# Performance work log

Hardware: AMD Instinct MI355X
Metric: run time of the kernel (lower is better)

Reference implementation:

```python
import jax, jax.numpy as jnp
import numpy as np

N_NODES = 50000
N_EDGES = 800000
F_IN = 2
T = 12
HID = 64
OUT = 12
K = 2  # diffusion order: identity + 1-hop (out- and in-directed)


def setup_inputs() -> dict:
    key = jax.random.key(0)
    ks = jax.random.split(key, 12)
    inp = {}
    inp["x"] = jax.random.normal(ks[0], (1, N_NODES, F_IN, T), dtype=jnp.float32)
    inp["edge_index"] = jax.random.randint(ks[1], (2, N_EDGES), 0, N_NODES)
    inp["edge_weight"] = jax.random.uniform(ks[2], (N_EDGES,), dtype=jnp.float32)

    def u(k, shape, fan):
        s = 1.0 / np.sqrt(fan)
        return jax.random.uniform(k, shape, jnp.float32, -s, s)

    c1 = F_IN + HID   # 66: DCRNN gates operate on cat([X, H])
    c2 = HID + HID    # 128
    inp["w1z"] = u(ks[3], (2, K, c1, HID), c1); inp["b1z"] = jnp.zeros((HID,), jnp.float32)
    inp["w1r"] = u(ks[4], (2, K, c1, HID), c1); inp["b1r"] = jnp.zeros((HID,), jnp.float32)
    inp["w1h"] = u(ks[5], (2, K, c1, HID), c1); inp["b1h"] = jnp.zeros((HID,), jnp.float32)
    inp["w2z"] = u(ks[6], (2, K, c2, HID), c2); inp["b2z"] = jnp.zeros((HID,), jnp.float32)
    inp["w2r"] = u(ks[7], (2, K, c2, HID), c2); inp["b2r"] = jnp.zeros((HID,), jnp.float32)
    inp["w2h"] = u(ks[8], (2, K, c2, HID), c2); inp["b2h"] = jnp.zeros((HID,), jnp.float32)
    inp["lin_w"] = u(ks[9], (HID, OUT), HID)
    inp["lin_b"] = u(ks[10], (OUT,), HID)
    return inp


def _dconv(X, row, col, norm_out, norm_in, w, b):
    # K=2 diffusion conv: H = X@W[:,0] + (D_O^-1 W diffusion)@W[0,1] + (D_I^-1 W^T diffusion)@W[1,1] + b
    H = X @ w[0, 0] + X @ w[1, 0]
    Xr = X[row]  # gather source-node features per edge: [E, C]
    Tx_o = jax.ops.segment_sum(norm_out[:, None] * Xr, col, num_segments=N_NODES)
    Tx_i = jax.ops.segment_sum(norm_in[:, None] * Xr, col, num_segments=N_NODES)
    return H + Tx_o @ w[0, 1] + Tx_i @ w[1, 1] + b


def _cell(X, H, row, col, no, ni, wz, bz, wr, br, wh, bh):
    # GRU-style DCRNN cell
    XH = jnp.concatenate([X, H], axis=1)
    Z = jax.nn.sigmoid(_dconv(XH, row, col, no, ni, wz, bz))
    R = jax.nn.sigmoid(_dconv(XH, row, col, no, ni, wr, br))
    Ht = jnp.tanh(_dconv(jnp.concatenate([X, R * H], axis=1), row, col, no, ni, wh, bh))
    return Z * H + (1.0 - Z) * Ht


def reference(x, edge_index, edge_weight, w1z, b1z, w1r, b1r, w1h, b1h,
              w2z, b2z, w2r, b2r, w2h, b2h, lin_w, lin_b):
    row, col = edge_index[0], edge_index[1]
    deg_out = jax.ops.segment_sum(edge_weight, row, num_segments=N_NODES)
    deg_in = jax.ops.segment_sum(edge_weight, col, num_segments=N_NODES)
    norm_out = edge_weight / deg_out[row]  # per-edge weight of D_O^{-1} W
    norm_in = edge_weight / deg_in[col]    # per-edge weight of D_I^{-1} W^T
    xs = jnp.transpose(x[0], (2, 0, 1))    # [T, N, F] (batch = 1)

    def step(carry, xt):
        h1, h2 = carry
        h1 = jax.nn.relu(_cell(xt, h1, row, col, norm_out, norm_in, w1z, b1z, w1r, b1r, w1h, b1h))
        h2 = jax.nn.relu(_cell(h1, h2, row, col, norm_out, norm_in, w2z, b2z, w2r, b2r, w2h, b2h))
        return (h1, h2), None

    h0 = jnp.zeros((N_NODES, HID), x.dtype)
    (h1, h2), _ = jax.lax.scan(step, (h0, h0), xs)
    out = h2 @ lin_w + lin_b  # [N, 12]
    return out.reshape(1, N_NODES, OUT)
```

## Files before the change

### kernel.cpp

```cpp
#include <hip/hip_runtime.h>

#define NN 50000
#define NE 800000
#define TT 12
#define NBIN (4 * NN)
#define NBLK ((NBIN + 255) / 256)

typedef _Float16 h16;
typedef __attribute__((ext_vector_type(2))) _Float16 h16x2;
typedef __attribute__((ext_vector_type(4))) _Float16 h16x4;
typedef __attribute__((ext_vector_type(8))) _Float16 half8;
typedef __attribute__((ext_vector_type(4))) float f32x4;
typedef __attribute__((address_space(3))) h16 as3h16;
typedef __attribute__((address_space(3))) half8 as3half8;

static constexpr size_t alignup(size_t x) { return (x + 255) & ~(size_t)255; }
static constexpr size_t O_CNT  = 0;
static constexpr size_t O_CUR  = alignup(O_CNT + NBIN + 1);
static constexpr size_t O_DEGO = alignup(O_CUR + NBIN);
static constexpr size_t O_BSUM = alignup(O_DEGO + NN);
static constexpr size_t O_BEXC = O_BSUM + 1024;
static constexpr size_t O_EDG  = alignup(O_BEXC + 1024);
static constexpr size_t O_TXX  = alignup(O_EDG + (size_t)NE * 2);
static constexpr size_t O_WF1ZR= alignup(O_TXX + (size_t)TT * NN * 4);
static constexpr size_t O_WF1H = alignup(O_WF1ZR + 12288);
static constexpr size_t O_WF2ZR= alignup(O_WF1H + 6144);
static constexpr size_t O_WF2H = alignup(O_WF2ZR + 24576);
static constexpr size_t O_WX1ZR= alignup(O_WF2H + 12288);
static constexpr size_t O_WX1H = alignup(O_WX1ZR + 768);
static constexpr size_t O_PX0  = alignup(O_WX1H + 384);
static constexpr size_t O_PX1  = O_PX0 + (size_t)NN * 64;
static constexpr size_t O_PZR  = O_PX1 + (size_t)NN * 64;
static constexpr size_t O_Z1   = O_PZR + (size_t)NN * 64;
static constexpr size_t O_Z2   = O_Z1 + (size_t)NN * 32;
static constexpr size_t O_TXA  = alignup(O_Z2 + (size_t)NN * 32);
static constexpr size_t O_TXB  = alignup(O_TXA + (size_t)NN * 64);
static constexpr size_t WS_FLOATS = O_TXB + (size_t)NN * 128;

__device__ __forceinline__ float sigm_(float x) { return 1.f / (1.f + __expf(-x)); }
__device__ __forceinline__ float tanh_(float x) { float e = __expf(2.f * x); return 1.f - 2.f / (e + 1.f); }

__device__ __forceinline__ void gld_lds16(const h16* g, as3h16* l) {
    __builtin_amdgcn_global_load_lds(
        (const __attribute__((address_space(1))) void*)g,
        (__attribute__((address_space(3))) void*)l, 16, 0, 0);
}

template <int N>
__device__ __forceinline__ void wait_lgkm0_vm() {
    if constexpr (N == 0)      asm volatile("s_waitcnt lgkmcnt(0) vmcnt(0)" ::: "memory");
    else if constexpr (N == 1) asm volatile("s_waitcnt lgkmcnt(0) vmcnt(1)" ::: "memory");
    else                       asm volatile("s_waitcnt lgkmcnt(0) vmcnt(2)" ::: "memory");
}


__global__ __launch_bounds__(256) void k_zero(float* ws) {
    size_t i = (size_t)blockIdx.x * 256 + threadIdx.x;
    size_t stride = (size_t)gridDim.x * 256;
    for (size_t p = i; p < O_BSUM + 2048; p += stride) ((int*)ws)[p] = 0;
    for (size_t p = i; p < (size_t)NN * 128; p += stride) ws[O_PX0 + p] = 0.f;
    for (size_t p = i; p < (size_t)NN * 128; p += stride) ws[O_TXB + p] = 0.f;
}

__global__ __launch_bounds__(256) void k_hist(const int* ei, float* ws) {
    int e = blockIdx.x * 256 + threadIdx.x;
    if (e >= NE) return;
    int r = ei[e], c = ei[NE + e];
    int bin = c * 4 + r / 12500;
    int rk = atomicAdd((int*)ws + O_CNT + bin, 1);
    ((int*)ws)[O_TXX + e] = rk;
}

__global__ __launch_bounds__(256) void k_scanA(float* ws) {
    __shared__ int sh[256];
    int t = threadIdx.x, i = blockIdx.x * 256 + t;
    int v = (i < NBIN) ? ((int*)ws)[O_CNT + i] : 0;
    sh[t] = v; __syncthreads();
    for (int o = 128; o > 0; o >>= 1) { if (t < o) sh[t] += sh[t + o]; __syncthreads(); }
    if (t == 0) ((int*)ws)[O_BSUM + blockIdx.x] = sh[0];
}

__global__ __launch_bounds__(256) void k_scanB(float* ws) {
    __shared__ int tot[256];
    int t = threadIdx.x;
    int* bsum = (int*)ws + O_BSUM;
    int* bexc = (int*)ws + O_BEXC;
    int base = t * 4;
    int v0 = (base + 0 < NBLK) ? bsum[base + 0] : 0;
    int v1 = (base + 1 < NBLK) ? bsum[base + 1] : 0;
    int v2 = (base + 2 < NBLK) ? bsum[base + 2] : 0;
    int v3 = (base + 3 < NBLK) ? bsum[base + 3] : 0;
    int sum = v0 + v1 + v2 + v3;
    tot[t] = sum; __syncthreads();
    for (int o = 1; o < 256; o <<= 1) {
        int a = (t >= o) ? tot[t - o] : 0;
        __syncthreads(); tot[t] += a; __syncthreads();
    }
    int excl = tot[t] - sum;
    if (base + 0 < NBLK) bexc[base + 0] = excl;
    if (base + 1 < NBLK) bexc[base + 1] = excl + v0;
    if (base + 2 < NBLK) bexc[base + 2] = excl + v0 + v1;
    if (base + 3 < NBLK) bexc[base + 3] = excl + v0 + v1 + v2;
    if (t == 255) ((int*)ws)[O_CNT + NBIN] = tot[255];
}

__global__ __launch_bounds__(256) void k_scanC(float* ws) {
    __shared__ int sh[256];
    int t = threadIdx.x, b = blockIdx.x, i = b * 256 + t;
    int v = (i < NBIN) ? ((int*)ws)[O_CNT + i] : 0;
    sh[t] = v; __syncthreads();
    for (int o = 1; o < 256; o <<= 1) {
        int a = (t >= o) ? sh[t - o] : 0;
        __syncthreads(); sh[t] += a; __syncthreads();
    }
    if (i < NBIN) ((int*)ws)[O_CNT + i] = ((int*)ws)[O_BEXC + b] + sh[t] - v;
}

__global__ __launch_bounds__(256) void k_scatter(const int* ei, const float* ew, float* ws) {
    int e = blockIdx.x * 256 + threadIdx.x;
    if (e >= NE) return;
    int r = ei[e], c = ei[NE + e];
    float w = ew[e];
    atomicAdd(ws + O_DEGO + r, w);
    int bin = c * 4 + r / 12500;
    int p = ((const int*)ws)[O_CNT + bin] + ((const int*)ws)[O_TXX + e];
    uint2 rec; rec.x = (unsigned)r; rec.y = __float_as_uint(w);
    ((uint2*)(ws + O_EDG))[p] = rec;
}

__global__ __launch_bounds__(256) void k_norm(float* ws) {
    int n = blockIdx.x * 4 + (threadIdx.x >> 6);
    int lane = threadIdx.x & 63;
    const int* offs = (const int*)ws + O_CNT;
    uint2* recs = (uint2*)(ws + O_EDG);
    const float* dego = ws + O_DEGO;
    int e0 = offs[4 * n], e1 = offs[4 * n + 4];
    float s = 0.f;
    for (int e = e0 + lane; e < e1; e += 64) s += __uint_as_float(recs[e].y);
    #pragma unroll
    for (int m = 1; m < 64; m <<= 1) s += __shfl_xor(s, m);
    float inv = 1.f / s;
    for (int e = e0 + lane; e < e1; e += 64) {
        uint2 r = recs[e];
        float w = __uint_as_float(r.y);
        h16x2 nv; nv.x = (h16)(w / dego[r.x]); nv.y = (h16)(w * inv);
        r.y = __builtin_bit_cast(unsigned int, nv);
        recs[e] = r;
    }
}

__global__ __launch_bounds__(256) void k_aggx(const float* __restrict__ x, float* __restrict__ ws) {
    int tid = threadIdx.x;
    int n = blockIdx.x * 8 + (tid >> 5);
    int l = tid & 31;
    const int* offs = (const int*)ws + O_CNT;
    const uint2* recs = (const uint2*)(ws + O_EDG);
    int e0 = offs[4 * n], e1 = offs[4 * n + 4];
    int f = l / 12, tt2 = l % 12;
    bool act = l < 24;
    float ao = 0.f, ai = 0.f;
    uint2 rc0, rc1;
    if (e0 < e1) {
        rc0 = recs[e0];
        rc1 = recs[(e0 + 1 < e1) ? e0 + 1 : e1 - 1];
    }
    for (int e = e0; e < e1; e += 2) {
        uint2 c0 = rc0, c1 = rc1;
        int n2 = (e + 2 < e1) ? e + 2 : e1 - 1, n3 = (e + 3 < e1) ? e + 3 : e1 - 1;
        rc0 = recs[n2]; rc1 = recs[n3];
        h16x2 nv0 = __builtin_bit_cast(h16x2, c0.y);
        h16x2 nv1 = __builtin_bit_cast(h16x2, c1.y);
        bool ok1 = (e + 1 < e1);
        float no1 = ok1 ? (float)nv1.x : 0.f, ni1 = ok1 ? (float)nv1.y : 0.f;
        if (act) {
            float v0 = x[(size_t)c0.x * 24 + f * 12 + tt2];
            float v1 = x[(size_t)c1.x * 24 + f * 12 + tt2];
            ao += (float)nv0.x * v0 + no1 * v1;
            ai += (float)nv0.y * v0 + ni1 * v1;
        }
    }
    if (act) {
        ws[O_TXX + ((size_t)tt2 * NN + n) * 4 + f] = ao;
        ws[O_TXX + ((size_t)tt2 * NN + n) * 4 + 2 + f] = ai;
    }
}

__device__ void packf_dev(int L, int NO, const float* wa, const float* wb, h16* Wf, int idx) {
    int C = (L == 1) ? 66 : 128;
    int NT = NO / 16;
    int j = idx & 7, l = (idx >> 3) & 63;
    int rest = idx >> 9;
    int ct = rest % NT, ks = rest / NT;
    int k = ks * 32 + ((l >> 4) << 3) + j;
    int col = ct * 16 + (l & 15);
    const float* w = wa; int jj = col;
    if (NO == 128 && col >= 64) { w = wb; jj = col - 64; }
    int G = k >> 6, c6 = k & 63, sg, crow;
    if (L == 1) { sg = G; crow = 2 + c6; }
    else        { sg = G >> 1; crow = ((G & 1) << 6) + c6; }
    float v;
    if (sg == 0)      v = w[(size_t)(0 * C + crow) * 64 + jj] + w[(size_t)(2 * C + crow) * 64 + jj];
    else if (sg == 1) v = w[(size_t)(1 * C + crow) * 64 + jj];
    else              v = w[(size_t)(3 * C + crow) * 64 + jj];
    Wf[idx] = (h16)v;
}

__device__ void packx_dev(int NO, const float* wa, const float* wb, float* Wx, int idx) {
    if (idx >= 6 * NO) return;
    int cc = idx / NO, col = idx % NO;
    const float* w = wa; int jj = col;
    if (NO == 128 && col >= 64) { w = wb; jj = col - 64; }
    int sg = cc >> 1, c = cc & 1;
    float v;
    if (sg == 0)      v = w[(size_t)(0 * 66 + c) * 64 + jj] + w[(size_t)(2 * 66 + c) * 64 + jj];
    else if (sg == 1) v = w[(size_t)(1 * 66 + c) * 64 + jj];
    else              v = w[(size_t)(3 * 66 + c) * 64 + jj];
    Wx[idx] = v;
}

__global__ __launch_bounds__(256) void k_packall(const float* w1z, const float* w1r, const float* w1h,
    const float* w2z, const float* w2r, const float* w2h, float* ws) {
    int b = blockIdx.x, t = threadIdx.x;
    if (b < 96)       packf_dev(1, 128, w1z, w1r, (h16*)(ws + O_WF1ZR), b * 256 + t);
    else if (b < 144) packf_dev(1, 64,  w1h, nullptr, (h16*)(ws + O_WF1H), (b - 96) * 256 + t);
    else if (b < 336) packf_dev(2, 128, w2z, w2r, (h16*)(ws + O_WF2ZR), (b - 144) * 256 + t);
    else if (b < 432) packf_dev(2, 64,  w2h, nullptr, (h16*)(ws + O_WF2H), (b - 336) * 256 + t);
    else {
        int idx = (b - 432) * 256 + t;
        if (idx < 768) packx_dev(128, w1z, w1r, ws + O_WX1ZR, idx);
        int idx2 = idx - 768;
        if (idx2 >= 0 && idx2 < 384) packx_dev(64, w1h, nullptr, ws + O_WX1H, idx2);
    }
}

__global__ __launch_bounds__(256) void k_aggP(
    const h16* __restrict__ T,
    h16* __restrict__ outA, int orsA, int oA, int iA,
    h16* __restrict__ outB, int orsB, int oB, int iB,
    const float* __restrict__ ws) {
    int tid = threadIdx.x, lane = tid & 63, wv = tid >> 6;
    int q = lane >> 4, fl = lane & 15;
    int n = blockIdx.x * 16 + wv * 4 + q;
    const int* offs = (const int*)ws + O_CNT;
    const uint2* recs = (const uint2*)(ws + O_EDG);
    int e0 = offs[4 * n], e1 = offs[4 * n + 4];
    float ao[8] = {}, ai[8] = {};
    for (int e = e0; e < e1; e += 4) {
        int i1 = e + 1 < e1 ? e + 1 : e1 - 1;
        int i2 = e + 2 < e1 ? e + 2 : e1 - 1;
        int i3 = e + 3 < e1 ? e + 3 : e1 - 1;
        uint2 r0 = recs[e], r1 = recs[i1], r2 = recs[i2], r3 = recs[i3];
        half8 v0 = *(const half8*)(T + (size_t)r0.x * 128 + fl * 8);
        half8 v1 = *(const half8*)(T + (size_t)r1.x * 128 + fl * 8);
        half8 v2 = *(const half8*)(T + (size_t)r2.x * 128 + fl * 8);
        half8 v3 = *(const half8*)(T + (size_t)r3.x * 128 + fl * 8);
        h16x2 m0 = __builtin_bit_cast(h16x2, r0.y);
        h16x2 m1 = __builtin_bit_cast(h16x2, r1.y);
        h16x2 m2 = __builtin_bit_cast(h16x2, r2.y);
        h16x2 m3 = __builtin_bit_cast(h16x2, r3.y);
        float no0 = (float)m0.x, ni0 = (float)m0.y;
        float no1 = (e + 1 < e1) ? (float)m1.x : 0.f, ni1 = (e + 1 < e1) ? (float)m1.y : 0.f;
        float no2 = (e + 2 < e1) ? (float)m2.x : 0.f, ni2 = (e + 2 < e1) ? (float)m2.y : 0.f;
        float no3 = (e + 3 < e1) ? (float)m3.x : 0.f, ni3 = (e + 3 < e1) ? (float)m3.y : 0.f;
        #pragma unroll
        for (int j = 0; j < 8; ++j) {
            float f0 = (float)v0[j], f1 = (float)v1[j], f2 = (float)v2[j], f3 = (float)v3[j];
            ao[j] += no0 * f0 + no1 * f1 + no2 * f2 + no3 * f3;
            ai[j] += ni0 * f0 + ni1 * f1 + ni2 * f2 + ni3 * f3;
        }
    }
    h16* outP = (fl < 8) ? outA : outB;
    int ors = (fl < 8) ? orsA : orsB;
    int fo = (fl < 8) ? fl : fl - 8;
    int oT = ((fl < 8) ? oA : oB) + fo * 8;
    int iT = ((fl < 8) ? iA : iB) + fo * 8;
    half8 wo, wi;
    #pragma unroll
    for (int j = 0; j < 8; ++j) { wo[j] = (h16)ao[j]; wi[j] = (h16)ai[j]; }
    *(half8*)(outP + (size_t)n * ors + oT) = wo;
    *(half8*)(outP + (size_t)n * ors + iT) = wi;
}

__global__ __launch_bounds__(256) void k_agg1(
    const h16* __restrict__ T, int hs,
    h16* __restrict__ out, int ors, int oA, int iA,
    const float* __restrict__ ws) {
    int tid = threadIdx.x, lane = tid & 63, wv = tid >> 6;
    int q = lane >> 3, fl = lane & 7;
    int n = blockIdx.x * 32 + wv * 8 + q;
    if (n >= NN) n = NN - 1;
    const int* offs = (const int*)ws + O_CNT;
    const uint2* recs = (const uint2*)(ws + O_EDG);
    int e0 = offs[4 * n], e1 = offs[4 * n + 4];
    float ao[8] = {}, ai[8] = {};
    for (int e = e0; e < e1; e += 2) {
        int i1 = e + 1 < e1 ? e + 1 : e1 - 1;
        uint2 r0 = recs[e], r1 = recs[i1];
        half8 v0 = *(const half8*)(T + (size_t)r0.x * hs + fl * 8);
        half8 v1 = *(const half8*)(T + (size_t)r1.x * hs + fl * 8);
        h16x2 m0 = __builtin_bit_cast(h16x2, r0.y);
        h16x2 m1 = __builtin_bit_cast(h16x2, r1.y);
        float no0 = (float)m0.x, ni0 = (float)m0.y;
        float no1 = (e + 1 < e1) ? (float)m1.x : 0.f, ni1 = (e + 1 < e1) ? (float)m1.y : 0.f;
        #pragma unroll
        for (int j = 0; j < 8; ++j) {
            float f0 = (float)v0[j], f1 = (float)v1[j];
            ao[j] += no0 * f0 + no1 * f1;
            ai[j] += ni0 * f0 + ni1 * f1;
        }
    }
    half8 wo, wi;
    #pragma unroll
    for (int j = 0; j < 8; ++j) { wo[j] = (h16)ao[j]; wi[j] = (h16)ai[j]; }
    *(half8*)(out + (size_t)n * ors + oA + fl * 8) = wo;
    *(half8*)(out + (size_t)n * ors + iA + fl * 8) = wi;
}

struct Seg { const h16* p[6]; int st[6]; int of[6]; };
#define RB ((NN + 63) / 64)

template <int G>
__device__ __forceinline__ void stage_g(as3h16* lds, const Seg& seg, int bi, int lane, int rh, int cq) {
    int r16 = lane & 15, kg = lane >> 4;
    int gr0 = bi * 64 + cq * 16 + r16; if (gr0 >= NN) gr0 = NN - 1;
    gld_lds16(seg.p[G] + (size_t)gr0 * seg.st[G] + seg.of[G] + rh * 32 + kg * 8,
              lds + (G & 3) * 4096 + (rh * 4 + cq) * 512);
}

template <int G, int NG, int CT>
__device__ __forceinline__ void gsteps(as3h16* lds, const Seg& seg, int bi, int lane, int rh, int cq,
                                       half8 (&wreg)[NG * 2][CT], f32x4 (&acc)[2][CT]) {
    if constexpr (G < NG) {
        constexpr int OUT = (NG - 1 - G) >= 2 ? 2 : (NG - 1 - G);
        wait_lgkm0_vm<OUT>();
        __builtin_amdgcn_s_barrier();
        asm volatile("" ::: "memory");
        if constexpr (G + 3 < NG) stage_g<G + 3>(lds, seg, bi, lane, rh, cq);
        #pragma unroll
        for (int kk = 0; kk < 2; ++kk) {
            half8 af[2];
            #pragma unroll
            for (int s = 0; s < 2; ++s)
                af[s] = *(const as3half8*)(lds + (G & 3) * 4096 + (kk * 4 + rh * 2 + s) * 512 + lane * 8);
            #pragma unroll
            for (int c = 0; c < CT; ++c)
                #pragma unroll
                for (int s = 0; s < 2; ++s)
                    acc[s][c] = __builtin_amdgcn_mfma_f32_16x16x32_f16(af[s], wreg[2 * G + kk][c], acc[s][c], 0, 0, 0);
        }
        gsteps<G + 1, NG, CT>(lds, seg, bi, lane, rh, cq, wreg, acc);
    }
}

template <int NG, int NO, int CT, int EPI, int XEPI>
__device__ __forceinline__ void mmg_body(int bi, const Seg& seg, const h16* __restrict__ Wf,
    const float* __restrict__ Wx, const float* __restrict__ x, const float* __restrict__ txx, int t,
    const float* __restrict__ Ba, const float* __restrict__ Bb,
    const h16* Hprev, h16* zbuf, h16* rhh, h16* houth, as3h16* lds) {
    constexpr int KS = NG * 2;
    constexpr int NT = NO / 16;
    int tid = threadIdx.x, lane = tid & 63, wv = tid >> 6;
    int cq = wv & 3, rh = wv >> 2;
    int ctb = cq * CT;
    int r16 = lane & 15;

    half8 wreg[KS][CT];
    #pragma unroll
    for (int ks = 0; ks < KS; ++ks)
        #pragma unroll
        for (int c = 0; c < CT; ++c)
            wreg[ks][c] = *(const half8*)(Wf + (((size_t)ks * NT + ctb + c) * 64 + lane) * 8);

    stage_g<0>(lds, seg, bi, lane, rh, cq);
    stage_g<1>(lds, seg, bi, lane, rh, cq);
    stage_g<2>(lds, seg, bi, lane, rh, cq);

    f32x4 acc[2][CT];
    #pragma unroll
    for (int s = 0; s < 2; ++s)
        #pragma unroll
        for (int c = 0; c < CT; ++c) acc[s][c] = (f32x4){0.f, 0.f, 0.f, 0.f};

    gsteps<0, NG, CT>(lds, seg, bi, lane, rh, cq, wreg, acc);

    int row0 = bi * 64 + rh * 32;
    int rg4 = (lane >> 4) * 4;
    #pragma unroll
    for (int s = 0; s < 2; ++s) {
        int rbase = row0 + s * 16 + rg4;
        float xa0[4], xa1[4]; float4 tg[4];
        if (XEPI) {
            #pragma unroll
            for (int r = 0; r < 4; ++r) {
                int row = rbase + r; if (row >= NN) row = NN - 1;
                xa0[r] = x[(size_t)row * 24 + t];
                xa1[r] = x[(size_t)row * 24 + 12 + t];
                tg[r] = *(const float4*)&txx[((size_t)t * NN + row) * 4];
            }
        }
        #pragma unroll
        for (int c = 0; c < CT; ++c) {
            int col = (ctb + c) * 16 + r16;
            float w0, w1, w2, w3, w4, w5;
            if (XEPI) {
                w0 = Wx[col]; w1 = Wx[NO + col]; w2 = Wx[2 * NO + col];
                w3 = Wx[3 * NO + col]; w4 = Wx[4 * NO + col]; w5 = Wx[5 * NO + col];
            }
            float bb = (EPI == 0) ? (col < 64 ? Ba[col] : Bb[col - 64]) : Ba[col];
            #pragma unroll
            for (int r = 0; r < 4; ++r) {
                int row = rbase + r;
                if (row >= NN) continue;
                float v = acc[s][c][r] + bb;
                if (XEPI) v += xa0[r] * w0 + xa1[r] * w1 + tg[r].x * w2 + tg[r].y * w3 + tg[r].z * w4 + tg[r].w * w5;
                if (EPI == 0) {
                    if (col < 64) zbuf[(size_t)row * 64 + col] = (h16)sigm_(v);
                    else {
                        float rr_ = sigm_(v);
                        float hp = (float)Hprev[(size_t)row * 128 + col - 64];
                        rhh[(size_t)row * 128 + col - 64] = (h16)(rr_ * hp);
                    }
                } else {
                    float ht = tanh_(v);
                    float z = (float)zbuf[(size_t)row * 64 + col];
                    float hp = (float)Hprev[(size_t)row * 128 + col];
                    float hn = fmaxf(z * hp + (1.f - z) * ht, 0.f);
                    houth[(size_t)row * 128 + col] = (h16)hn;
                }
            }
        }
    }
}

template <int NG, int NO, int CT, int EPI, int XEPI>
__global__ __launch_bounds__(512, 2) void k_mmg(Seg seg, const h16* __restrict__ Wf,
    const float* __restrict__ Wx, const float* __restrict__ x, const float* __restrict__ txx, int t,
    const float* __restrict__ Ba, const float* __restrict__ Bb,
    const h16* Hprev, h16* zbuf, h16* rhh, h16* houth) {
    __shared__ __align__(16) h16 smem[4 * 4096];
    mmg_body<NG, NO, CT, EPI, XEPI>(blockIdx.x, seg, Wf, Wx, x, txx, t, Ba, Bb, Hprev, zbuf, rhh, houth,
                                    (as3h16*)smem);
}

__global__ __launch_bounds__(512, 2) void k_mmzr2(Seg sA, Seg sB,
    const h16* __restrict__ wfA, const h16* __restrict__ wfB, const float* __restrict__ wxB,
    const float* __restrict__ x, const float* __restrict__ txx, int tB,
    const float* __restrict__ bAz, const float* __restrict__ bAr,
    const float* __restrict__ bBz, const float* __restrict__ bBr,
    const h16* hpA, h16* zA, h16* rhA,
    const h16* hpB, h16* zB, h16* rhB) {
    __shared__ __align__(16) h16 smem[4 * 4096];
    if (blockIdx.x < RB)
        mmg_body<6, 128, 2, 0, 0>(blockIdx.x, sA, wfA, nullptr, nullptr, nullptr, 0, bAz, bAr,
                                  hpA, zA, rhA, nullptr, (as3h16*)smem);
    else
        mmg_body<3, 128, 2, 0, 1>(blockIdx.x - RB, sB, wfB, wxB, x, txx, tB, bBz, bBr,
                                  hpB, zB, rhB, nullptr, (as3h16*)smem);
}

__global__ __launch_bounds__(512, 2) void k_mmh2(Seg sA, Seg sB,
    const h16* __restrict__ wfA, const h16* __restrict__ wfB, const float* __restrict__ wxB,
    const float* __restrict__ x, const float* __restrict__ txx, int tB,
    const float* __restrict__ bAh, const float* __restrict__ bBh,
    h16* zA, const h16* hpA, h16* hoA,
    h16* zB, const h16* hpB, h16* hoB) {
    __shared__ __align__(16) h16 smem[4 * 4096];
    if (blockIdx.x < RB)
        mmg_body<6, 64, 1, 1, 0>(blockIdx.x, sA, wfA, nullptr, nullptr, nullptr, 0, bAh, nullptr,
                                 hpA, zA, nullptr, hoA, (as3h16*)smem);
    else
        mmg_body<3, 64, 1, 1, 1>(blockIdx.x - RB, sB, wfB, wxB, x, txx, tB, bBh, nullptr,
                                 hpB, zB, nullptr, hoB, (as3h16*)smem);
}

__global__ __launch_bounds__(256) void k_final(const h16* __restrict__ h2p, const float* __restrict__ lw,
                                               const float* __restrict__ lb, float* __restrict__ out) {
    __shared__ float sh[16 * 65];
    int t = threadIdx.x;
    int n0 = blockIdx.x * 16;
    int idx = t * 4;
    int nl = idx >> 6, h = idx & 63;
    h16x4 v = *(const h16x4*)&h2p[(size_t)(n0 + nl) * 128 + h];
    sh[nl * 65 + h] = (float)v[0]; sh[nl * 65 + h + 1] = (float)v[1];
    sh[nl * 65 + h + 2] = (float)v[2]; sh[nl * 65 + h + 3] = (float)v[3];
    __syncthreads();
    if (t < 192) {
        int n = t / 12, o = t % 12;
        float acc = lb[o];
        #pragma unroll 8
        for (int k = 0; k < 64; ++k) acc += sh[n * 65 + k] * lw[k * 12 + o];
        out[(size_t)(n0 + n) * 12 + o] = acc;
    }
}

extern "C" void kernel_launch(void* const* d_in, const int* in_sizes, int n_in,
                              void* d_out, int out_size, void* d_ws, size_t ws_size,
                              hipStream_t stream) {
    const float* x   = (const float*)d_in[0];
    const int*   ei  = (const int*)d_in[1];
    const float* ew  = (const float*)d_in[2];
    const float* w1z = (const float*)d_in[3];  const float* b1z = (const float*)d_in[4];
    const float* w1r = (const float*)d_in[5];  const float* b1r = (const float*)d_in[6];
    const float* w1h = (const float*)d_in[7];  const float* b1h = (const float*)d_in[8];
    const float* w2z = (const float*)d_in[9];  const float* b2z = (const float*)d_in[10];
    const float* w2r = (const float*)d_in[11]; const float* b2r = (const float*)d_in[12];
    const float* w2h = (const float*)d_in[13]; const float* b2h = (const float*)d_in[14];
    const float* lw  = (const float*)d_in[15]; const float* lb  = (const float*)d_in[16];
    float* out = (float*)d_out;
    float* ws  = (float*)d_ws;
    if (ws_size < WS_FLOATS * sizeof(float)) return;

    k_zero<<<2048, 256, 0, stream>>>(ws);
    k_hist<<<(NE + 255) / 256, 256, 0, stream>>>(ei, ws);
    k_scanA<<<NBLK, 256, 0, stream>>>(ws);
    k_scanB<<<1, 256, 0, stream>>>(ws);
    k_scanC<<<NBLK, 256, 0, stream>>>(ws);
    k_scatter<<<(NE + 255) / 256, 256, 0, stream>>>(ei, ew, ws);
    k_norm<<<NN / 4, 256, 0, stream>>>(ws);
    k_aggx<<<NN / 8, 256, 0, stream>>>(x, ws);
    k_packall<<<437, 256, 0, stream>>>(w1z, w1r, w1h, w2z, w2r, w2h, ws);

    h16* pEven = (h16*)(ws + O_PX0);
    h16* pOdd  = (h16*)(ws + O_PX1);
    h16* pzr   = (h16*)(ws + O_PZR);
    h16* z1    = (h16*)(ws + O_Z1);
    h16* z2    = (h16*)(ws + O_Z2);
    h16* txA = (h16*)(ws + O_TXA);
    h16* txB = (h16*)(ws + O_TXB);
    const float* txx = ws + O_TXX;
    const h16* wf1zr = (const h16*)(ws + O_WF1ZR);
    const h16* wf1h  = (const h16*)(ws + O_WF1H);
    const h16* wf2zr = (const h16*)(ws + O_WF2ZR);
    const h16* wf2h  = (const h16*)(ws + O_WF2H);
    const float* wx1zr = ws + O_WX1ZR;
    const float* wx1h  = ws + O_WX1H;
    const int GAP = NN / 16;
    const int GA1 = (NN + 31) / 32;

    auto s1zr = [&](h16* px) -> Seg {
        return {{px, txB, txB, nullptr, nullptr, nullptr}, {128, 256, 256, 0, 0, 0}, {0, 0, 128, 0, 0, 0}};
    };
    Seg s1h = {{pzr, txA, txA, nullptr, nullptr, nullptr}, {128, 128, 128, 0, 0, 0}, {0, 0, 64, 0, 0, 0}};
    auto s2zr = [&](h16* px) -> Seg {
        return {{px, px, txB, txB, txB, txB}, {128, 128, 256, 256, 256, 256}, {0, 64, 0, 64, 128, 192}};
    };
    auto s2h = [&](h16* px) -> Seg {
        return {{px, pzr, txB, txB, txB, txB}, {128, 128, 256, 256, 256, 256}, {0, 64, 0, 64, 128, 192}};
    };

    k_mmg<3, 128, 2, 0, 1><<<RB, 512, 0, stream>>>(s1zr(pOdd), wf1zr, wx1zr, x, txx, 0,
        b1z, b1r, pOdd, z1, pzr, nullptr);
    k_agg1<<<GA1, 256, 0, stream>>>(pzr, 128, txA, 128, 0, 64, ws);
    k_mmg<3, 64, 1, 1, 1><<<RB, 512, 0, stream>>>(s1h, wf1h, wx1h, x, txx, 0,
        b1h, nullptr, pOdd, z1, nullptr, pEven);
    k_aggP<<<GAP, 256, 0, stream>>>(pEven, txB, 256, 0, 128, txB, 256, 64, 192, ws);

    for (int t = 0; t < TT - 1; ++t) {
        h16* pxT  = (t & 1) ? pOdd : pEven;
        h16* pxT1 = (t & 1) ? pEven : pOdd;
        k_mmzr2<<<RB * 2, 512, 0, stream>>>(s2zr(pxT), s1zr(pxT), wf2zr, wf1zr, wx1zr,
            x, txx, t + 1, b2z, b2r, b1z, b1r,
            pxT + 64, z2, pzr + 64,
            pxT,      z1, pzr);
        k_aggP<<<GAP, 256, 0, stream>>>(pzr, txA, 128, 0, 64, txB, 256, 64, 192, ws);
        k_mmh2<<<RB * 2, 512, 0, stream>>>(s2h(pxT), s1h, wf2h, wf1h, wx1h,
            x, txx, t + 1, b2h, b1h,
            z2, pxT + 64, pxT1 + 64,
            z1, pxT,      pxT1);
        k_aggP<<<GAP, 256, 0, stream>>>(pxT1, txB, 256, 0, 128, txB, 256, 64, 192, ws);
    }

    k_mmg<6, 128, 2, 0, 0><<<RB, 512, 0, stream>>>(s2zr(pOdd), wf2zr, nullptr, nullptr, nullptr, 0,
        b2z, b2r, pOdd + 64, z2, pzr + 64, nullptr);
    k_agg1<<<GA1, 256, 0, stream>>>(pzr + 64, 128, txB, 256, 64, 192, ws);
    k_mmg<6, 64, 1, 1, 0><<<RB, 512, 0, stream>>>(s2h(pOdd), wf2h, nullptr, nullptr, nullptr, 0,
        b2h, nullptr, pOdd + 64, z2, nullptr, pEven + 64);
    k_final<<<NN / 16, 256, 0, stream>>>(pEven + 64, lw, lb, out);
}
```

Baseline: 1.695 ms.

## Widen edge gather to 8 in flight and split preprocessing launches

The aggregation kernel now loads 8 edge records and 8 neighbor feature vectors per iteration instead of 4, so more memory loads are outstanding per wave, at the cost of extra registers. The histogram and scatter preprocessing kernels are each split into two launches over the two halves of the edge list, which adds launch overhead and has no clear speed purpose. A register variable is also hoisted earlier in the matmul body.

```diff
diff --git a/kernel.cpp b/kernel.cpp
--- a/kernel.cpp
+++ b/kernel.cpp
@@ -5,6 +5,7 @@
 #define TT 12
 #define NBIN (4 * NN)
 #define NBLK ((NBIN + 255) / 256)
+#define EHALF (NE / 2)
 
 typedef _Float16 h16;
 typedef __attribute__((ext_vector_type(2))) _Float16 h16x2;
@@ -62,9 +63,9 @@
     for (size_t p = i; p < (size_t)NN * 128; p += stride) ws[O_TXB + p] = 0.f;
 }
 
-__global__ __launch_bounds__(256) void k_hist(const int* ei, float* ws) {
-    int e = blockIdx.x * 256 + threadIdx.x;
-    if (e >= NE) return;
+__global__ __launch_bounds__(256) void k_hist(const int* ei, float* ws, int ebase) {
+    int e = ebase + blockIdx.x * 256 + threadIdx.x;
+    if (e >= NE || e >= ebase + EHALF) return;
     int r = ei[e], c = ei[NE + e];
     int bin = c * 4 + r / 12500;
     int rk = atomicAdd((int*)ws + O_CNT + bin, 1);
@@ -116,9 +117,9 @@
     if (i < NBIN) ((int*)ws)[O_CNT + i] = ((int*)ws)[O_BEXC + b] + sh[t] - v;
 }
 
-__global__ __launch_bounds__(256) void k_scatter(const int* ei, const float* ew, float* ws) {
-    int e = blockIdx.x * 256 + threadIdx.x;
-    if (e >= NE) return;
+__global__ __launch_bounds__(256) void k_scatter(const int* ei, const float* ew, float* ws, int ebase) {
+    int e = ebase + blockIdx.x * 256 + threadIdx.x;
+    if (e >= NE || e >= ebase + EHALF) return;
     int r = ei[e], c = ei[NE + e];
     float w = ew[e];
     atomicAdd(ws + O_DEGO + r, w);
@@ -245,28 +246,25 @@
     const uint2* recs = (const uint2*)(ws + O_EDG);
     int e0 = offs[4 * n], e1 = offs[4 * n + 4];
     float ao[8] = {}, ai[8] = {};
-    for (int e = e0; e < e1; e += 4) {
-        int i1 = e + 1 < e1 ? e + 1 : e1 - 1;
-        int i2 = e + 2 < e1 ? e + 2 : e1 - 1;
-        int i3 = e + 3 < e1 ? e + 3 : e1 - 1;
-        uint2 r0 = recs[e], r1 = recs[i1], r2 = recs[i2], r3 = recs[i3];
-        half8 v0 = *(const half8*)(T + (size_t)r0.x * 128 + fl * 8);
-        half8 v1 = *(const half8*)(T + (size_t)r1.x * 128 + fl * 8);
-        half8 v2 = *(const half8*)(T + (size_t)r2.x * 128 + fl * 8);
-        half8 v3 = *(const half8*)(T + (size_t)r3.x * 128 + fl * 8);
-        h16x2 m0 = __builtin_bit_cast(h16x2, r0.y);
-        h16x2 m1 = __builtin_bit_cast(h16x2, r1.y);
-        h16x2 m2 = __builtin_bit_cast(h16x2, r2.y);
-        h16x2 m3 = __builtin_bit_cast(h16x2, r3.y);
-        float no0 = (float)m0.x, ni0 = (float)m0.y;
-        float no1 = (e + 1 < e1) ? (float)m1.x : 0.f, ni1 = (e + 1 < e1) ? (float)m1.y : 0.f;
-        float no2 = (e + 2 < e1) ? (float)m2.x : 0.f, ni2 = (e + 2 < e1) ? (float)m2.y : 0.f;
-        float no3 = (e + 3 < e1) ? (float)m3.x : 0.f, ni3 = (e + 3 < e1) ? (float)m3.y : 0.f;
+    for (int e = e0; e < e1; e += 8) {
+        uint2 rr[8];
+        #pragma unroll
+        for (int j = 0; j < 8; ++j) { int i = (e + j < e1) ? e + j : e1 - 1; rr[j] = recs[i]; }
+        half8 vv[8];
+        #pragma unroll
+        for (int j = 0; j < 8; ++j) vv[j] = *(const half8*)(T + (size_t)rr[j].x * 128 + fl * 8);
         #pragma unroll
         for (int j = 0; j < 8; ++j) {
-            float f0 = (float)v0[j], f1 = (float)v1[j], f2 = (float)v2[j], f3 = (float)v3[j];
-            ao[j] += no0 * f0 + no1 * f1 + no2 * f2 + no3 * f3;
-            ai[j] += ni0 * f0 + ni1 * f1 + ni2 * f2 + ni3 * f3;
+            h16x2 m = __builtin_bit_cast(h16x2, rr[j].y);
+            bool ok = (j == 0) || (e + j < e1);
+            float no = ok ? (float)m.x : 0.f;
+            float ni = ok ? (float)m.y : 0.f;
+            #pragma unroll
+            for (int k = 0; k < 8; ++k) {
+                float f = (float)vv[j][k];
+                ao[k] += no * f;
+                ai[k] += ni * f;
+            }
         }
     }
     h16* outP = (fl < 8) ? outA : outB;
@@ -363,6 +361,7 @@
     int cq = wv & 3, rh = wv >> 2;
     int ctb = cq * CT;
     int r16 = lane & 15;
+    int rg4 = (lane >> 4) * 4;
 
     half8 wreg[KS][CT];
     #pragma unroll
@@ -384,7 +383,6 @@
     gsteps<0, NG, CT>(lds, seg, bi, lane, rh, cq, wreg, acc);
 
     int row0 = bi * 64 + rh * 32;
-    int rg4 = (lane >> 4) * 4;
     #pragma unroll
     for (int s = 0; s < 2; ++s) {
         int rbase = row0 + s * 16 + rg4;
@@ -510,12 +508,15 @@
     float* ws  = (float*)d_ws;
     if (ws_size < WS_FLOATS * sizeof(float)) return;
 
+    const int EHB = (EHALF + 255) / 256;
     k_zero<<<2048, 256, 0, stream>>>(ws);
-    k_hist<<<(NE + 255) / 256, 256, 0, stream>>>(ei, ws);
+    k_hist<<<EHB, 256, 0, stream>>>(ei, ws, 0);
+    k_hist<<<EHB, 256, 0, stream>>>(ei, ws, EHALF);
     k_scanA<<<NBLK, 256, 0, stream>>>(ws);
     k_scanB<<<1, 256, 0, stream>>>(ws);
     k_scanC<<<NBLK, 256, 0, stream>>>(ws);
-    k_scatter<<<(NE + 255) / 256, 256, 0, stream>>>(ei, ew, ws);
+    k_scatter<<<EHB, 256, 0, stream>>>(ei, ew, ws, 0);
+    k_scatter<<<EHB, 256, 0, stream>>>(ei, ew, ws, EHALF);
     k_norm<<<NN / 4, 256, 0, stream>>>(ws);
     k_aggx<<<NN / 8, 256, 0, stream>>>(x, ws);
     k_packall<<<437, 256, 0, stream>>>(w1z, w1r, w1h, w2z, w2r, w2h, ws);
```

Result: no change. 1.709 ms (+0.9%).
